# Performance work log

Hardware: AMD Instinct MI355X
Metric: run time of the kernel (lower is better)

## Reference

```python
import jax, jax.numpy as jnp
import numpy as np

B = 16          # batch (number of point clouds)
N = 16384       # total points across batch
H = 512         # hidden_size
E = 64          # traj_embed_size
T = 8           # max_traj_len
EB = 72         # euler_bins = 360 // 5
OUT = EB * 3 + 2  # action_mlp output: 216 rot logits + open + stop = 218
TEMP = 1.0


def setup_inputs() -> dict:
    key = jax.random.key(0)
    ks = jax.random.split(key, 8)
    rng = np.random.default_rng(0)
    # ragged segment sizes, each >= 256, summing exactly to N
    counts = rng.multinomial(N - B * 256, np.ones(B) / B) + 256
    s = 0.02
    return {
        "point_embeds": jax.random.normal(ks[0], (N, H), jnp.float32),
        "coords": jax.random.normal(ks[1], (N, 3), jnp.float32),
        "traj_emb": jax.random.normal(ks[2], (T, E), jnp.float32) * s,
        "hm_w1": jax.random.normal(ks[3], (H + E, H), jnp.float32) * s,
        "hm_b1": jnp.zeros((H,), jnp.float32),
        "hm_w2": jax.random.normal(ks[4], (H, 4), jnp.float32) * s,
        "hm_b2": jnp.zeros((4,), jnp.float32),
        "act_w1": jax.random.normal(ks[5], (H + E, H), jnp.float32) * s,
        "act_b1": jnp.zeros((H,), jnp.float32),
        "act_w2": jax.random.normal(ks[6], (H, OUT), jnp.float32) * s,
        "act_b2": jnp.zeros((OUT,), jnp.float32),
        "npoints_in_batch": jnp.asarray(counts, jnp.int32),
    }


def _lrelu(x):
    return jnp.where(x >= 0, x, 0.02 * x)


def reference(point_embeds, coords, traj_emb, hm_w1, hm_b1, hm_w2, hm_b2,
              act_w1, act_b1, act_w2, act_b2, npoints_in_batch):
    n = point_embeds.shape[0]
    # segment id per point (replaces torch.split over ragged batch)
    seg = jnp.repeat(jnp.arange(B), npoints_in_batch, total_repeat_length=n)  # (N,)

    # expand with trajectory-step embedding: (N, T, H+E)
    pe = jnp.concatenate([
        jnp.broadcast_to(point_embeds[:, None, :], (n, T, H)),
        jnp.broadcast_to(traj_emb[None, :, :], (n, T, E)),
    ], axis=-1)

    # heatmap MLP: (N, T, 4) = [heatmap logit, delta xyz]
    hm = _lrelu(pe @ hm_w1 + hm_b1) @ hm_w2 + hm_b2
    logits = hm[..., 0]                                # (N, T)

    # per-segment stable softmax over points
    m = jax.ops.segment_max(logits, seg, num_segments=B)          # (B, T)
    e = jnp.exp((logits - m[seg]) / TEMP)                         # (N, T)
    z = jax.ops.segment_sum(e, seg, num_segments=B)               # (B, T)
    h = e / z[seg]                                                # (N, T)

    new_coords = coords[:, None, :] + hm[..., 1:]                 # (N, T, 3)
    xt = jax.ops.segment_sum(h[..., None] * new_coords, seg, num_segments=B)  # (B, T, 3)

    # reduce == 'max': per-segment max pooling of point embeds
    pc = jax.ops.segment_max(pe, seg, num_segments=B)             # (B, T, H+E)
    ae = _lrelu(pc @ act_w1 + act_b1) @ act_w2 + act_b2           # (B, T, 218)

    xr = ae[..., :EB * 3].reshape(B, T, EB, 3)  # euler_disc logits
    xo = ae[..., -2]
    xstop = ae[..., -1]
    return (xt, xr, xo, xstop)
```

## Files before the change

### kernel.cpp

```cpp
#include <hip/hip_runtime.h>
#include <math.h>

typedef unsigned short u16;
typedef unsigned int u32;

#define NPTS 16384
#define HID  512
#define TT   8
#define TE   64
#define NB   16
#define OUTC 218

typedef short s16x8 __attribute__((ext_vector_type(8)));
typedef float f32x4 __attribute__((ext_vector_type(4)));

__device__ __forceinline__ float bf2f(u16 u) {
  return __uint_as_float(((u32)u) << 16);
}
__device__ __forceinline__ u16 f2bf(float f) {
  u32 x = __float_as_uint(f);
  x += 0x7fffu + ((x >> 16) & 1u);
  return (u16)(x >> 16);
}
__device__ __forceinline__ float lrelu(float h) { return fmaxf(h, 0.02f * h); }

__device__ __forceinline__ float rd(const void* p, size_t i, bool f32) {
  return f32 ? ((const float*)p)[i] : bf2f(((const u16*)p)[i]);
}
__device__ __forceinline__ void wr(void* p, size_t i, bool f32, float v) {
  if (f32) ((float*)p)[i] = v;
  else ((u16*)p)[i] = f2bf(v);
}

__device__ __forceinline__ void split_bf16(float x, u16& hi, u16& lo) {
  const u32 xu = __float_as_uint(x);
  hi = (u16)(xu >> 16);
  const float rem = x - __uint_as_float(xu & 0xffff0000u);
  lo = f2bf(rem);
}

__global__ __launch_bounds__(256) void sniff_kernel(const u16* __restrict__ pe,
                                                    int* __restrict__ flag) {
  __shared__ int s;
  const int tid = threadIdx.x;
  if (tid == 0) s = 0;
  __syncthreads();
  int c = 0;
  for (int i = tid; i < 8192; i += 256) {
    const u16 v = pe[i];
    if ((v & 0x7F80u) == 0x7F80u) c = 1;
  }
  if (c) s = 1;
  __syncthreads();
  if (tid == 0) flag[0] = s;
}

__global__ __launch_bounds__(256) void prep_kernel(
    const void* __restrict__ hm_w1, const void* __restrict__ hm_b1,
    const void* __restrict__ traj, const void* __restrict__ hm_w2,
    const void* __restrict__ hm_b2, const void* __restrict__ aw1,
    const void* __restrict__ ab1, float* __restrict__ vprime,
    float* __restrict__ w2f, float* __restrict__ b2f,
    float* __restrict__ avp, const int* __restrict__ flag) {
  const bool f32 = flag[0] != 0;
  const int tid = threadIdx.x, blk = blockIdx.x;
  if (blk < 8) {
    const int t = blk;
    for (int j = tid; j < 512; j += 256) {
      float acc = rd(hm_b1, j, f32);
      for (int e = 0; e < 64; ++e)
        acc = fmaf(rd(traj, t * 64 + e, f32),
                   rd(hm_w1, (size_t)(512 + e) * 512 + j, f32), acc);
      vprime[t * 512 + j] = acc;
    }
  } else if (blk < 16) {
    const int t = blk - 8;
    for (int j = tid; j < 512; j += 256) {
      float acc = rd(ab1, j, f32);
      for (int e = 0; e < 64; ++e)
        acc = fmaf(rd(traj, t * 64 + e, f32),
                   rd(aw1, (size_t)(512 + e) * 512 + j, f32), acc);
      avp[t * 512 + j] = acc;
    }
  } else {
    for (int i = tid; i < 2048; i += 256) w2f[i] = rd(hm_w2, i, f32);
    if (tid < 4) b2f[tid] = rd(hm_b2, tid, f32);
  }
}

__global__ __launch_bounds__(256) void conv_w1_kernel(
    const float* __restrict__ W1, u16* __restrict__ Bth, u16* __restrict__ Btl,
    const int* __restrict__ flag) {
  if (flag[0] == 0) return;
  const int g = blockIdx.x * 256 + threadIdx.x;
  const int j = g & 511;
  const int kbase = (g >> 9) * 8;
  s16x8 hv, lv;
#pragma unroll
  for (int i = 0; i < 8; ++i) {
    u16 h, l;
    split_bf16(W1[(size_t)(kbase + i) * 512 + j], h, l);
    hv[i] = (short)h;
    lv[i] = (short)l;
  }
  const int seg = (j >> 4) * 16 + (kbase >> 5);
  const int lane_ = (((kbase >> 3) & 3) << 4) | (j & 15);
  const size_t dst = ((size_t)seg * 64 + lane_) * 8;
  *(s16x8*)&Bth[dst] = hv;
  *(s16x8*)&Btl[dst] = lv;
}

#define SU_STRIDE 516
__global__ __launch_bounds__(256, 2) void gemm_fused(
    const float* __restrict__ A, const u16* __restrict__ Bth,
    const u16* __restrict__ Btl, const float* __restrict__ vprime,
    const float* __restrict__ w2f, const float* __restrict__ b2f,
    const float* __restrict__ coords, float* __restrict__ logits,
    float* __restrict__ nc, const int* __restrict__ flag) {
  if (flag[0] == 0) return;
  __shared__ __attribute__((aligned(16))) char smem[32 * SU_STRIDE * 4];
  u16* sAh = (u16*)smem;
  u16* sAl = (u16*)(smem + 32768);
  const int tid = threadIdx.x;
  const int rb = blockIdx.x * 32;
  for (int c = tid; c < 2048; c += 256) {
    const int row = c >> 6;
    const int kc = c & 63;
    const float* src = A + (size_t)(rb + row) * 512 + kc * 8;
    const float4 x0 = *(const float4*)(src);
    const float4 x1 = *(const float4*)(src + 4);
    const float xs[8] = {x0.x, x0.y, x0.z, x0.w, x1.x, x1.y, x1.z, x1.w};
    s16x8 hv, lv;
#pragma unroll
    for (int i = 0; i < 8; ++i) {
      u16 h, l;
      split_bf16(xs[i], h, l);
      hv[i] = (short)h;
      lv[i] = (short)l;
    }
    const int kstep = kc >> 2, kg = kc & 3;
    const int seg = (row >> 4) * 16 + kstep;
    const int lane_ = (kg << 4) | (row & 15);
    const int dst = (seg * 64 + lane_) * 8;
    *(s16x8*)&sAh[dst] = hv;
    *(s16x8*)&sAl[dst] = lv;
  }
  __syncthreads();
  const int wave = tid >> 6, lane = tid & 63;
  const int colT0 = wave * 8;
  f32x4 acc[2][8];
#pragma unroll
  for (int rt = 0; rt < 2; ++rt)
#pragma unroll
    for (int ct = 0; ct < 8; ++ct) acc[rt][ct] = (f32x4){0.f, 0.f, 0.f, 0.f};
#pragma unroll 1
  for (int kstep = 0; kstep < 16; ++kstep) {
    s16x8 ah[2], al[2], bh[8], bl[8];
#pragma unroll
    for (int rt = 0; rt < 2; ++rt) {
      const int off = ((rt * 16 + kstep) * 64 + lane) * 8;
      ah[rt] = *(const s16x8*)&sAh[off];
      al[rt] = *(const s16x8*)&sAl[off];
    }
#pragma unroll
    for (int ct = 0; ct < 8; ++ct) {
      const size_t boff = (((size_t)(colT0 + ct) * 16 + kstep) * 64 + lane) * 8;
      bh[ct] = *(const s16x8*)&Bth[boff];
      bl[ct] = *(const s16x8*)&Btl[boff];
    }
#pragma unroll
    for (int rt = 0; rt < 2; ++rt)
#pragma unroll
      for (int ct = 0; ct < 8; ++ct) {
        acc[rt][ct] = __builtin_amdgcn_mfma_f32_16x16x32_bf16(
            ah[rt], bh[ct], acc[rt][ct], 0, 0, 0);
        acc[rt][ct] = __builtin_amdgcn_mfma_f32_16x16x32_bf16(
            ah[rt], bl[ct], acc[rt][ct], 0, 0, 0);
        acc[rt][ct] = __builtin_amdgcn_mfma_f32_16x16x32_bf16(
            al[rt], bh[ct], acc[rt][ct], 0, 0, 0);
      }
  }
  __syncthreads();
  float* sU = (float*)smem;
  const int lr = lane & 15, orow = (lane >> 4) * 4;
#pragma unroll
  for (int rt = 0; rt < 2; ++rt)
#pragma unroll
    for (int ct = 0; ct < 8; ++ct) {
      const int col = wave * 128 + ct * 16 + lr;
#pragma unroll
      for (int r = 0; r < 4; ++r)
        sU[(rt * 16 + orow + r) * SU_STRIDE + col] = acc[rt][ct][r];
    }
  __syncthreads();
  const int ln = tid >> 3, t = tid & 7;
  const int n = rb + ln;
  const float* su = sU + ln * SU_STRIDE;
  const float* vp = vprime + t * 512;
  const float4* w4 = (const float4*)w2f;
  float a0 = 0.f, a1 = 0.f, a2 = 0.f, a3 = 0.f;
#pragma unroll 4
  for (int j4 = 0; j4 < 128; ++j4) {
    const float4 uu = *(const float4*)(su + j4 * 4);
    const float4 vv = *(const float4*)(vp + j4 * 4);
    const float4 w_0 = w4[j4 * 4 + 0];
    const float4 w_1 = w4[j4 * 4 + 1];
    const float4 w_2 = w4[j4 * 4 + 2];
    const float4 w_3 = w4[j4 * 4 + 3];
    float h;
    h = lrelu(uu.x + vv.x);
    a0 = fmaf(h, w_0.x, a0); a1 = fmaf(h, w_0.y, a1);
    a2 = fmaf(h, w_0.z, a2); a3 = fmaf(h, w_0.w, a3);
    h = lrelu(uu.y + vv.y);
    a0 = fmaf(h, w_1.x, a0); a1 = fmaf(h, w_1.y, a1);
    a2 = fmaf(h, w_1.z, a2); a3 = fmaf(h, w_1.w, a3);
    h = lrelu(uu.z + vv.z);
    a0 = fmaf(h, w_2.x, a0); a1 = fmaf(h, w_2.y, a1);
    a2 = fmaf(h, w_2.z, a2); a3 = fmaf(h, w_2.w, a3);
    h = lrelu(uu.w + vv.w);
    a0 = fmaf(h, w_3.x, a0); a1 = fmaf(h, w_3.y, a1);
    a2 = fmaf(h, w_3.z, a2); a3 = fmaf(h, w_3.w, a3);
  }
  logits[(size_t)n * 8 + t] = a0 + b2f[0];
  float* o = nc + ((size_t)n * 8 + t) * 3;
  o[0] = coords[(size_t)n * 3 + 0] + a1 + b2f[1];
  o[1] = coords[(size_t)n * 3 + 1] + a2 + b2f[2];
  o[2] = coords[(size_t)n * 3 + 2] + a3 + b2f[3];
}

#define GR 16
#define KBODY                                                                  \
  _Pragma("unroll") for (int r = 0; r < GR; ++r) {                             \
    const float4 a = *(const float4*)&sA[r * 512 + k];                         \
    acc0[r] = fmaf(a.x, w0[0],                                                 \
              fmaf(a.y, w0[1], fmaf(a.z, w0[2], fmaf(a.w, w0[3], acc0[r])))); \
    acc1[r] = fmaf(a.x, w1[0],                                                 \
              fmaf(a.y, w1[1], fmaf(a.z, w1[2], fmaf(a.w, w1[3], acc1[r])))); \
  }

__global__ __launch_bounds__(256) void gemm_naive(
    const void* __restrict__ A, const void* __restrict__ W1,
    float* __restrict__ U, const int* __restrict__ flag) {
  const bool f32 = flag[0] != 0;
  if (f32) return;
  __shared__ float sA[GR * 512];
  const int tid = threadIdx.x;
  const int rb = blockIdx.x * GR;
  for (int i = tid; i < GR * 512; i += 256) {
    const int r = i >> 9, k = i & 511;
    sA[i] = rd(A, (size_t)(rb + r) * 512 + k, f32);
  }
  __syncthreads();
  const int j0 = tid, j1 = tid + 256;
  float acc0[GR], acc1[GR];
#pragma unroll
  for (int r = 0; r < GR; ++r) { acc0[r] = 0.f; acc1[r] = 0.f; }
  {
    const u16* W = (const u16*)W1;
    for (int k = 0; k < 512; k += 4) {
      float w0[4], w1[4];
#pragma unroll
      for (int kk = 0; kk < 4; ++kk) {
        w0[kk] = bf2f(W[(size_t)(k + kk) * 512 + j0]);
        w1[kk] = bf2f(W[(size_t)(k + kk) * 512 + j1]);
      }
      KBODY
    }
  }
#pragma unroll
  for (int r = 0; r < GR; ++r) {
    U[(size_t)(rb + r) * 512 + j0] = acc0[r];
    U[(size_t)(rb + r) * 512 + j1] = acc1[r];
  }
}

__global__ __launch_bounds__(256) void segmax_kernel(
    const void* __restrict__ pe, const int* __restrict__ npts,
    float* __restrict__ partial, const int* __restrict__ flag) {
  const bool f32 = flag[0] != 0;
  const int blk = blockIdx.x;
  const int b = blk >> 4, c = blk & 15;
  int s0 = 0, cnt = 0;
  for (int i = 0; i < 16; ++i) {
    const int v = npts[i];
    if (i < b) s0 += v;
    if (i == b) cnt = v;
  }
  const int chunk = (cnt + 15) >> 4;
  const int r0 = s0 + c * chunk;
  int r1 = r0 + chunk;
  const int rend = s0 + cnt;
  if (r1 > rend) r1 = rend;
  const int j2 = threadIdx.x;
  float m0 = -1e30f, m1 = -1e30f;
  if (f32) {
    const float* pf = (const float*)pe;
    for (int n = r0; n < r1; ++n) {
      const float2 v = *(const float2*)(pf + (size_t)n * 512 + 2 * j2);
      m0 = fmaxf(m0, v.x);
      m1 = fmaxf(m1, v.y);
    }
  } else {
    const u32* p32 = (const u32*)pe;
    for (int n = r0; n < r1; ++n) {
      const u32 v = p32[(size_t)n * 256 + j2];
      m0 = fmaxf(m0, bf2f((u16)(v & 0xffffu)));
      m1 = fmaxf(m1, bf2f((u16)(v >> 16)));
    }
  }
  partial[(size_t)blk * 512 + 2 * j2] = m0;
  partial[(size_t)blk * 512 + 2 * j2 + 1] = m1;
}

__global__ __launch_bounds__(256) void stage2_kernel(
    const float* __restrict__ U, const float* __restrict__ vprime,
    const float* __restrict__ w2f, const float* __restrict__ b2f,
    const void* __restrict__ coords, float* __restrict__ logits,
    float* __restrict__ nc, const int* __restrict__ flag) {
  const bool f32 = flag[0] != 0;
  if (f32) return;
  __shared__ float s_vp[TT * 512];
  const int tid = threadIdx.x;
  for (int i = tid; i < TT * 512; i += 256) s_vp[i] = vprime[i];
  __syncthreads();
  const int g = (blockIdx.x << 8) + tid;
  const int n = g >> 3, t = g & 7;
  const float4* u4 = (const float4*)(U + (size_t)n * 512);
  const float4* v4 = (const float4*)(s_vp + t * 512);
  const float4* w4 = (const float4*)w2f;
  float a0 = 0.f, a1 = 0.f, a2 = 0.f, a3 = 0.f;
  for (int j4 = 0; j4 < 128; ++j4) {
    const float4 uu = u4[j4];
    const float4 vv = v4[j4];
    const float4 w_0 = w4[j4 * 4 + 0];
    const float4 w_1 = w4[j4 * 4 + 1];
    const float4 w_2 = w4[j4 * 4 + 2];
    const float4 w_3 = w4[j4 * 4 + 3];
    float h;
    h = lrelu(uu.x + vv.x);
    a0 = fmaf(h, w_0.x, a0); a1 = fmaf(h, w_0.y, a1);
    a2 = fmaf(h, w_0.z, a2); a3 = fmaf(h, w_0.w, a3);
    h = lrelu(uu.y + vv.y);
    a0 = fmaf(h, w_1.x, a0); a1 = fmaf(h, w_1.y, a1);
    a2 = fmaf(h, w_1.z, a2); a3 = fmaf(h, w_1.w, a3);
    h = lrelu(uu.z + vv.z);
    a0 = fmaf(h, w_2.x, a0); a1 = fmaf(h, w_2.y, a1);
    a2 = fmaf(h, w_2.z, a2); a3 = fmaf(h, w_2.w, a3);
    h = lrelu(uu.w + vv.w);
    a0 = fmaf(h, w_3.x, a0); a1 = fmaf(h, w_3.y, a1);
    a2 = fmaf(h, w_3.z, a2); a3 = fmaf(h, w_3.w, a3);
  }
  logits[g] = a0 + b2f[0];
  float* o = nc + (size_t)g * 3;
  o[0] = rd(coords, (size_t)n * 3 + 0, f32) + a1 + b2f[1];
  o[1] = rd(coords, (size_t)n * 3 + 1, f32) + a2 + b2f[2];
  o[2] = rd(coords, (size_t)n * 3 + 2, f32) + a3 + b2f[3];
}

__global__ __launch_bounds__(256) void softmax_xt_kernel(
    const float* __restrict__ logits, const float* __restrict__ nc,
    const int* __restrict__ npts, void* __restrict__ out,
    const int* __restrict__ flag) {
  const bool f32 = flag[0] != 0;
  const int b = blockIdx.x >> 3, t = blockIdx.x & 7;
  const int tid = threadIdx.x;
  int s0 = 0, cnt = 0;
  for (int i = 0; i < 16; ++i) {
    const int v = npts[i];
    if (i < b) s0 += v;
    if (i == b) cnt = v;
  }
  __shared__ float wm[4];
  __shared__ float red[4][4];
  float m = -1e30f;
  for (int i = tid; i < cnt; i += 256)
    m = fmaxf(m, logits[(size_t)(s0 + i) * 8 + t]);
#pragma unroll
  for (int o = 32; o > 0; o >>= 1) m = fmaxf(m, __shfl_down(m, o, 64));
  if ((tid & 63) == 0) wm[tid >> 6] = m;
  __syncthreads();
  const float mt = fmaxf(fmaxf(wm[0], wm[1]), fmaxf(wm[2], wm[3]));
  float z = 0.f, x = 0.f, y = 0.f, w = 0.f;
  for (int i = tid; i < cnt; i += 256) {
    const size_t g = (size_t)(s0 + i) * 8 + t;
    const float e = expf(logits[g] - mt);
    const float* c3 = nc + g * 3;
    z += e;
    x = fmaf(e, c3[0], x);
    y = fmaf(e, c3[1], y);
    w = fmaf(e, c3[2], w);
  }
#pragma unroll
  for (int o = 32; o > 0; o >>= 1) {
    z += __shfl_down(z, o, 64);
    x += __shfl_down(x, o, 64);
    y += __shfl_down(y, o, 64);
    w += __shfl_down(w, o, 64);
  }
  if ((tid & 63) == 0) {
    red[0][tid >> 6] = z; red[1][tid >> 6] = x;
    red[2][tid >> 6] = y; red[3][tid >> 6] = w;
  }
  __syncthreads();
  if (tid == 0) {
    const float Z = red[0][0] + red[0][1] + red[0][2] + red[0][3];
    const float X = red[1][0] + red[1][1] + red[1][2] + red[1][3];
    const float Y = red[2][0] + red[2][1] + red[2][2] + red[2][3];
    const float W = red[3][0] + red[3][1] + red[3][2] + red[3][3];
    wr(out, (size_t)(b * 8 + t) * 3 + 0, f32, X / Z);
    wr(out, (size_t)(b * 8 + t) * 3 + 1, f32, Y / Z);
    wr(out, (size_t)(b * 8 + t) * 3 + 2, f32, W / Z);
  }
}

__global__ __launch_bounds__(256) void act_hid_kernel(
    const float* __restrict__ partial, const void* __restrict__ aw1,
    const float* __restrict__ avp, float* __restrict__ hid,
    const int* __restrict__ flag) {
  const bool f32 = flag[0] != 0;
  const int b = blockIdx.x >> 3, jt = blockIdx.x & 7;
  __shared__ float spc[512];
  __shared__ float sred[4][64];
  const int tid = threadIdx.x;
  for (int k = tid; k < 512; k += 256) {
    float m = -1e30f;
#pragma unroll
    for (int c = 0; c < 16; ++c)
      m = fmaxf(m, partial[(size_t)(b * 16 + c) * 512 + k]);
    spc[k] = m;
  }
  __syncthreads();
  const int jj = tid & 63, kq = tid >> 6;
  const int j = jt * 64 + jj;
  const int kb = kq * 128;
  float a0 = 0.f, a1 = 0.f, a2 = 0.f, a3 = 0.f;
  if (f32) {
    const float* W = (const float*)aw1 + (size_t)kb * 512 + j;
#pragma unroll 4
    for (int k = 0; k < 128; k += 4) {
      a0 = fmaf(spc[kb + k + 0], W[(size_t)(k + 0) * 512], a0);
      a1 = fmaf(spc[kb + k + 1], W[(size_t)(k + 1) * 512], a1);
      a2 = fmaf(spc[kb + k + 2], W[(size_t)(k + 2) * 512], a2);
      a3 = fmaf(spc[kb + k + 3], W[(size_t)(k + 3) * 512], a3);
    }
  } else {
    const u16* W = (const u16*)aw1 + (size_t)kb * 512 + j;
#pragma unroll 4
    for (int k = 0; k < 128; k += 4) {
      a0 = fmaf(spc[kb + k + 0], bf2f(W[(size_t)(k + 0) * 512]), a0);
      a1 = fmaf(spc[kb + k + 1], bf2f(W[(size_t)(k + 1) * 512]), a1);
      a2 = fmaf(spc[kb + k + 2], bf2f(W[(size_t)(k + 2) * 512]), a2);
      a3 = fmaf(spc[kb + k + 3], bf2f(W[(size_t)(k + 3) * 512]), a3);
    }
  }
  sred[kq][jj] = (a0 + a1) + (a2 + a3);
  __syncthreads();
  if (kq == 0) {
    const float s = (sred[0][jj] + sred[1][jj]) + (sred[2][jj] + sred[3][jj]);
#pragma unroll
    for (int t = 0; t < 8; ++t)
      hid[(size_t)(b * 8 + t) * 512 + j] = lrelu(s + avp[t * 512 + j]);
  }
}

__global__ __launch_bounds__(256) void act_out_kernel(
    const float* __restrict__ hid, const void* __restrict__ aw2,
    const void* __restrict__ ab2, void* __restrict__ out,
    const int* __restrict__ flag) {
  const bool f32 = flag[0] != 0;
  __shared__ float sh[512];
  const int row = blockIdx.x, tid = threadIdx.x;
  for (int i = tid; i < 512; i += 256) sh[i] = hid[(size_t)row * 512 + i];
  __syncthreads();
  if (tid < OUTC) {
    float a0 = 0.f, a1 = 0.f, a2 = 0.f, a3 = 0.f;
    if (f32) {
      const float* W = (const float*)aw2 + tid;
#pragma unroll 8
      for (int j = 0; j < 512; j += 4) {
        a0 = fmaf(sh[j + 0], W[(size_t)(j + 0) * OUTC], a0);
        a1 = fmaf(sh[j + 1], W[(size_t)(j + 1) * OUTC], a1);
        a2 = fmaf(sh[j + 2], W[(size_t)(j + 2) * OUTC], a2);
        a3 = fmaf(sh[j + 3], W[(size_t)(j + 3) * OUTC], a3);
      }
    } else {
      const u16* W = (const u16*)aw2 + tid;
#pragma unroll 8
      for (int j = 0; j < 512; j += 4) {
        a0 = fmaf(sh[j + 0], bf2f(W[(size_t)(j + 0) * OUTC]), a0);
        a1 = fmaf(sh[j + 1], bf2f(W[(size_t)(j + 1) * OUTC]), a1);
        a2 = fmaf(sh[j + 2], bf2f(W[(size_t)(j + 2) * OUTC]), a2);
        a3 = fmaf(sh[j + 3], bf2f(W[(size_t)(j + 3) * OUTC]), a3);
      }
    }
    const float o = rd(ab2, tid, f32) + ((a0 + a1) + (a2 + a3));
    if (tid < 216)
      wr(out, 384 + (size_t)row * 216 + tid, f32, o);
    else if (tid == 216)
      wr(out, 384 + 27648 + row, f32, o);
    else
      wr(out, 384 + 27648 + 128 + row, f32, o);
  }
}

extern "C" void kernel_launch(void* const* d_in, const int* in_sizes, int n_in,
                              void* d_out, int out_size, void* d_ws,
                              size_t ws_size, hipStream_t stream) {
  (void)in_sizes; (void)n_in; (void)out_size; (void)ws_size;
  const void* pe     = d_in[0];
  const void* coords = d_in[1];
  const void* traj   = d_in[2];
  const void* hm_w1  = d_in[3];
  const void* hm_b1  = d_in[4];
  const void* hm_w2  = d_in[5];
  const void* hm_b2  = d_in[6];
  const void* aw1    = d_in[7];
  const void* ab1    = d_in[8];
  const void* aw2    = d_in[9];
  const void* ab2    = d_in[10];
  const int* npts    = (const int*)d_in[11];

  char* ws = (char*)d_ws;
  int*   flag    = (int*)(ws + 0);
  float* avp     = (float*)(ws + 256);
  float* hid     = (float*)(ws + 16896);
  float* U       = (float*)(ws + 524288);
  float* vprime  = (float*)(ws + 34078720);
  float* w2f     = (float*)(ws + 34095104);
  float* b2f     = (float*)(ws + 34103296);
  float* logits  = (float*)(ws + 34103552);
  float* nc      = (float*)(ws + 34627840);
  float* partial = (float*)(ws + 36200704);
  u16*   Bth     = (u16*)(ws + 524288);
  u16*   Btl     = (u16*)(ws + 524288 + 524288);

  sniff_kernel<<<1, 256, 0, stream>>>((const u16*)pe, flag);
  prep_kernel<<<17, 256, 0, stream>>>(hm_w1, hm_b1, traj, hm_w2, hm_b2,
                                      aw1, ab1, vprime, w2f, b2f, avp, flag);
  conv_w1_kernel<<<128, 256, 0, stream>>>((const float*)hm_w1, Bth, Btl, flag);
  gemm_fused<<<NPTS / 32, 256, 0, stream>>>((const float*)pe, Bth, Btl,
                                            vprime, w2f, b2f,
                                            (const float*)coords, logits, nc,
                                            flag);
  gemm_naive<<<NPTS / GR, 256, 0, stream>>>(pe, hm_w1, U, flag);
  segmax_kernel<<<256, 256, 0, stream>>>(pe, npts, partial, flag);
  stage2_kernel<<<512, 256, 0, stream>>>(U, vprime, w2f, b2f, coords, logits,
                                         nc, flag);
  softmax_xt_kernel<<<128, 256, 0, stream>>>(logits, nc, npts, d_out, flag);
  act_hid_kernel<<<128, 256, 0, stream>>>(partial, aw1, avp, hid, flag);
  act_out_kernel<<<128, 256, 0, stream>>>(hid, aw2, ab2, d_out, flag);
}
```

Before: 210.5 us.

## Double gemm_fused threads to 512 with split column tiles and split-K epilogue reduction

Runs the fused heatmap GEMM with 512 threads per block, so each wave covers 4 column tiles instead of 8. This cuts accumulator registers and raises the occupancy hint. The A staging loop is rewritten so each thread writes its MFMA-layout slot directly and loads stay coalesced. The second-layer epilogue is split across two halves of the hidden dimension and combined through a shared-memory reduction. The cost is an extra barrier and the shared reduction buffer, and each block reads B more redundantly per output.

```diff
diff --git a/kernel.cpp b/kernel.cpp
--- a/kernel.cpp
+++ b/kernel.cpp
@@ -111,7 +111,7 @@
 }
 
 #define SU_STRIDE 516
-__global__ __launch_bounds__(256, 2) void gemm_fused(
+__global__ __launch_bounds__(512, 4) void gemm_fused(
     const float* __restrict__ A, const u16* __restrict__ Bth,
     const u16* __restrict__ Btl, const float* __restrict__ vprime,
     const float* __restrict__ w2f, const float* __restrict__ b2f,
@@ -119,13 +119,16 @@
     float* __restrict__ nc, const int* __restrict__ flag) {
   if (flag[0] == 0) return;
   __shared__ __attribute__((aligned(16))) char smem[32 * SU_STRIDE * 4];
+  __shared__ float4 sred[256];
   u16* sAh = (u16*)smem;
   u16* sAl = (u16*)(smem + 32768);
   const int tid = threadIdx.x;
   const int rb = blockIdx.x * 32;
-  for (int c = tid; c < 2048; c += 256) {
-    const int row = c >> 6;
-    const int kc = c & 63;
+#pragma unroll
+  for (int it = 0; it < 4; ++it) {
+    const int c = tid + it * 512;
+    const int row = ((c >> 10) << 4) | (c & 15);
+    const int kc = (((c >> 6) & 15) << 2) | ((c >> 4) & 3);
     const float* src = A + (size_t)(rb + row) * 512 + kc * 8;
     const float4 x0 = *(const float4*)(src);
     const float4 x1 = *(const float4*)(src + 4);
@@ -138,24 +141,26 @@
       hv[i] = (short)h;
       lv[i] = (short)l;
     }
-    const int kstep = kc >> 2, kg = kc & 3;
-    const int seg = (row >> 4) * 16 + kstep;
-    const int lane_ = (kg << 4) | (row & 15);
-    const int dst = (seg * 64 + lane_) * 8;
-    *(s16x8*)&sAh[dst] = hv;
-    *(s16x8*)&sAl[dst] = lv;
+    *(s16x8*)&sAh[c * 8] = hv;
+    *(s16x8*)&sAl[c * 8] = lv;
   }
   __syncthreads();
   const int wave = tid >> 6, lane = tid & 63;
-  const int colT0 = wave * 8;
-  f32x4 acc[2][8];
+  const int colT0 = wave * 4;
+  f32x4 acc[2][4];
 #pragma unroll
   for (int rt = 0; rt < 2; ++rt)
 #pragma unroll
-    for (int ct = 0; ct < 8; ++ct) acc[rt][ct] = (f32x4){0.f, 0.f, 0.f, 0.f};
+    for (int ct = 0; ct < 4; ++ct) acc[rt][ct] = (f32x4){0.f, 0.f, 0.f, 0.f};
 #pragma unroll 1
   for (int kstep = 0; kstep < 16; ++kstep) {
-    s16x8 ah[2], al[2], bh[8], bl[8];
+    s16x8 ah[2], al[2], bh[4], bl[4];
+#pragma unroll
+    for (int ct = 0; ct < 4; ++ct) {
+      const size_t boff = (((size_t)(colT0 + ct) * 16 + kstep) * 64 + lane) * 8;
+      bh[ct] = *(const s16x8*)&Bth[boff];
+      bl[ct] = *(const s16x8*)&Btl[boff];
+    }
 #pragma unroll
     for (int rt = 0; rt < 2; ++rt) {
       const int off = ((rt * 16 + kstep) * 64 + lane) * 8;
@@ -163,15 +168,9 @@
       al[rt] = *(const s16x8*)&sAl[off];
     }
 #pragma unroll
-    for (int ct = 0; ct < 8; ++ct) {
-      const size_t boff = (((size_t)(colT0 + ct) * 16 + kstep) * 64 + lane) * 8;
-      bh[ct] = *(const s16x8*)&Bth[boff];
-      bl[ct] = *(const s16x8*)&Btl[boff];
-    }
-#pragma unroll
     for (int rt = 0; rt < 2; ++rt)
 #pragma unroll
-      for (int ct = 0; ct < 8; ++ct) {
+      for (int ct = 0; ct < 4; ++ct) {
         acc[rt][ct] = __builtin_amdgcn_mfma_f32_16x16x32_bf16(
             ah[rt], bh[ct], acc[rt][ct], 0, 0, 0);
         acc[rt][ct] = __builtin_amdgcn_mfma_f32_16x16x32_bf16(
@@ -186,21 +185,22 @@
 #pragma unroll
   for (int rt = 0; rt < 2; ++rt)
 #pragma unroll
-    for (int ct = 0; ct < 8; ++ct) {
-      const int col = wave * 128 + ct * 16 + lr;
+    for (int ct = 0; ct < 4; ++ct) {
+      const int col = wave * 64 + ct * 16 + lr;
 #pragma unroll
       for (int r = 0; r < 4; ++r)
         sU[(rt * 16 + orow + r) * SU_STRIDE + col] = acc[rt][ct][r];
     }
   __syncthreads();
-  const int ln = tid >> 3, t = tid & 7;
+  const int p = tid & 255, half = tid >> 8;
+  const int ln = p >> 3, t = p & 7;
   const int n = rb + ln;
-  const float* su = sU + ln * SU_STRIDE;
-  const float* vp = vprime + t * 512;
-  const float4* w4 = (const float4*)w2f;
+  const float* su = sU + ln * SU_STRIDE + half * 256;
+  const float* vp = vprime + t * 512 + half * 256;
+  const float4* w4 = (const float4*)w2f + half * 256;
   float a0 = 0.f, a1 = 0.f, a2 = 0.f, a3 = 0.f;
 #pragma unroll 4
-  for (int j4 = 0; j4 < 128; ++j4) {
+  for (int j4 = 0; j4 < 64; ++j4) {
     const float4 uu = *(const float4*)(su + j4 * 4);
     const float4 vv = *(const float4*)(vp + j4 * 4);
     const float4 w_0 = w4[j4 * 4 + 0];
@@ -221,11 +221,17 @@
     a0 = fmaf(h, w_3.x, a0); a1 = fmaf(h, w_3.y, a1);
     a2 = fmaf(h, w_3.z, a2); a3 = fmaf(h, w_3.w, a3);
   }
-  logits[(size_t)n * 8 + t] = a0 + b2f[0];
-  float* o = nc + ((size_t)n * 8 + t) * 3;
-  o[0] = coords[(size_t)n * 3 + 0] + a1 + b2f[1];
-  o[1] = coords[(size_t)n * 3 + 1] + a2 + b2f[2];
-  o[2] = coords[(size_t)n * 3 + 2] + a3 + b2f[3];
+  if (half) sred[p] = make_float4(a0, a1, a2, a3);
+  __syncthreads();
+  if (!half) {
+    const float4 r = sred[p];
+    a0 += r.x; a1 += r.y; a2 += r.z; a3 += r.w;
+    logits[(size_t)n * 8 + t] = a0 + b2f[0];
+    float* o = nc + ((size_t)n * 8 + t) * 3;
+    o[0] = coords[(size_t)n * 3 + 0] + a1 + b2f[1];
+    o[1] = coords[(size_t)n * 3 + 1] + a2 + b2f[2];
+    o[2] = coords[(size_t)n * 3 + 2] + a3 + b2f[3];
+  }
 }
 
 #define GR 16
@@ -538,7 +544,7 @@
   prep_kernel<<<17, 256, 0, stream>>>(hm_w1, hm_b1, traj, hm_w2, hm_b2,
                                       aw1, ab1, vprime, w2f, b2f, avp, flag);
   conv_w1_kernel<<<128, 256, 0, stream>>>((const float*)hm_w1, Bth, Btl, flag);
-  gemm_fused<<<NPTS / 32, 256, 0, stream>>>((const float*)pe, Bth, Btl,
+  gemm_fused<<<NPTS / 32, 512, 0, stream>>>((const float*)pe, Bth, Btl,
                                             vprime, w2f, b2f,
                                             (const float*)coords, logits, nc,
                                             flag);
```

Measured after the change: 241.5 us. +14.8%, slower.
